# Kernel tuning notes

Hardware: AMD Instinct MI355X
Metric: run time of the kernel (lower is better)

The kernel has to match this reference:

```python
import jax, jax.numpy as jnp
import numpy as np

B, S, D = 4, 2048, 1024
H = 16
DH = D // H          # 64
DFF = 4096
EPS = 1e-5


def _layer_norm(x, gamma, beta):
    mu = jnp.mean(x, axis=-1, keepdims=True)
    var = jnp.mean(jnp.square(x - mu), axis=-1, keepdims=True)
    return (x - mu) * jax.lax.rsqrt(var + EPS) * gamma + beta


def setup_inputs() -> dict:
    key = jax.random.key(0)
    ks = jax.random.split(key, 8)
    s_in = 1.0 / np.sqrt(D)
    s_ff = 1.0 / np.sqrt(DFF)
    return {
        "x": jax.random.normal(ks[0], (B, S, D), dtype=jnp.float32),
        # per-head qkv weights stacked: [H, D, 3*DH] (nn.Linear, bias=False)
        "Wqkv": jax.random.normal(ks[1], (H, D, 3 * DH), dtype=jnp.float32) * s_in,
        "Wproj": jax.random.normal(ks[2], (D, D), dtype=jnp.float32) * s_in,
        "bproj": jnp.zeros((D,), dtype=jnp.float32),
        "ln1_g": jnp.ones((D,), dtype=jnp.float32),
        "ln1_b": jnp.zeros((D,), dtype=jnp.float32),
        "ln2_g": jnp.ones((D,), dtype=jnp.float32),
        "ln2_b": jnp.zeros((D,), dtype=jnp.float32),
        "W1": jax.random.normal(ks[3], (D, DFF), dtype=jnp.float32) * s_in,
        "b1": jnp.zeros((DFF,), dtype=jnp.float32),
        "W2": jax.random.normal(ks[4], (DFF, D), dtype=jnp.float32) * s_ff,
        "b2": jnp.zeros((D,), dtype=jnp.float32),
    }


def reference(x, Wqkv, Wproj, bproj, ln1_g, ln1_b, ln2_g, ln2_b, W1, b1, W2, b2):
    # fused multi-head QKV projection: [B,S,D] x [H,D,3*DH] -> [B,H,S,3*DH]
    qkv = jnp.einsum('bsd,hde->bhse', x, Wqkv)
    q, k, v = jnp.split(qkv, 3, axis=-1)          # each [B,H,S,DH]
    scale = 1.0 / jnp.sqrt(jnp.asarray(DH, dtype=x.dtype))
    scores = jnp.einsum('bhsd,bhtd->bhst', q, k) * scale   # [B,H,S,S]
    causal = jnp.tril(jnp.ones((S, S), dtype=bool))
    scores = jnp.where(causal, scores, jnp.finfo(x.dtype).min)
    attn = jax.nn.softmax(scores, axis=-1)
    heads = jnp.einsum('bhst,bhtd->bhsd', attn, v)          # [B,H,S,DH]
    att_out = heads.transpose(0, 2, 1, 3).reshape(B, S, D)  # concat heads
    att_out = att_out @ Wproj + bproj
    out = _layer_norm(x + att_out, ln1_g, ln1_b)            # dropout = identity (eval)
    mlp_out = (jax.nn.gelu(out @ W1 + b1, approximate=False)) @ W2 + b2
    out = _layer_norm(out + mlp_out, ln2_g, ln2_b)
    return out
```

## Files before the change

kernel.cpp:

```cpp
#include <hip/hip_runtime.h>
#include <math.h>

#define BB 4
#define SS 2048
#define DD 1024
#define HH 16
#define DHH 64
#define DFF 4096
static constexpr float LN_EPS = 1e-5f;

typedef __bf16 bf16x8 __attribute__((ext_vector_type(8)));
typedef float f32x4 __attribute__((ext_vector_type(4)));
typedef unsigned short u16x8 __attribute__((ext_vector_type(8)));

__device__ inline unsigned short f2bf(float f) {
    union { float f; unsigned int u; } v; v.f = f;
    unsigned int u = v.u + 0x7FFFu + ((v.u >> 16) & 1u);
    return (unsigned short)(u >> 16);
}

__device__ __forceinline__ float fexp2(float x) {
    return __builtin_amdgcn_exp2f(x);
}

__device__ __forceinline__ void gl_lds16(const unsigned short* g,
                                         unsigned short* l) {
    __builtin_amdgcn_global_load_lds(
        (const __attribute__((address_space(1))) unsigned int*)g,
        (__attribute__((address_space(3))) unsigned int*)l, 16, 0, 0);
}

__global__ __launch_bounds__(256) void transpose_bf16_kernel(
    const float* __restrict__ in, unsigned short* __restrict__ outT,
    int R, int C) {
    __shared__ float t[64][65];
    const int r0 = blockIdx.y * 64, c0 = blockIdx.x * 64;
    const int cl = threadIdx.x & 63, rl = threadIdx.x >> 6;
#pragma unroll
    for (int rr = 0; rr < 16; ++rr)
        t[rl + rr * 4][cl] = in[(size_t)(r0 + rl + rr * 4) * C + c0 + cl];
    __syncthreads();
#pragma unroll
    for (int rr = 0; rr < 16; ++rr)
        outT[(size_t)(c0 + rl + rr * 4) * R + r0 + cl] = f2bf(t[cl][rl + rr * 4]);
}

__global__ __launch_bounds__(256) void repack_wqkv_bf16_kernel(
    const float* __restrict__ Wqkv, unsigned short* __restrict__ Wq2T) {
    __shared__ float t[64][65];
    const int h = blockIdx.z;
    const int d0 = blockIdx.y * 64, e0 = blockIdx.x * 64;
    const int cl = threadIdx.x & 63, rl = threadIdx.x >> 6;
#pragma unroll
    for (int rr = 0; rr < 16; ++rr)
        t[rl + rr * 4][cl] =
            Wqkv[((size_t)h * DD + d0 + rl + rr * 4) * 192 + e0 + cl];
    __syncthreads();
#pragma unroll
    for (int rr = 0; rr < 16; ++rr)
        Wq2T[((size_t)h * 192 + e0 + rl + rr * 4) * DD + d0 + cl] =
            f2bf(t[cl][rl + rr * 4]);
}

__global__ __launch_bounds__(256) void f2bf_kernel(
    const float* __restrict__ in, unsigned short* __restrict__ out, int n) {
    int i = blockIdx.x * 256 + threadIdx.x;
    if (i < n) out[i] = f2bf(in[i]);
}

template <int MODE>
__global__ __launch_bounds__(256) void mfma_gemm_kernel(
    const unsigned short* __restrict__ A, const unsigned short* __restrict__ BT,
    float* __restrict__ Cf, unsigned short* __restrict__ Cb,
    const float* __restrict__ bias, const float* __restrict__ resid,
    unsigned short* __restrict__ Qb, unsigned short* __restrict__ Kb,
    unsigned short* __restrict__ VTb, int M, int N, int K) {
    __shared__ __align__(16) unsigned short lds_g[128 * 32 * 2];
    unsigned short* Als = lds_g;
    unsigned short* Bls = lds_g + 128 * 32;
    const int tid = threadIdx.x;
    const int lane = tid & 63;
    const int wave = tid >> 6;
    const int wr = (wave >> 1) * 64;
    const int wc = (wave & 1) * 64;
    const int row0 = blockIdx.y * 128;
    const int col0 = blockIdx.x * 128;

    const int lr = tid >> 2;
    const int lsl = (tid & 3) * 8;
    const int lkg = (((tid & 3) ^ ((lr >> 1) & 3)) * 8);
    const int l15 = lane & 15;
    const int g = lane >> 4;
    const int fk = ((g ^ ((l15 >> 1) & 3)) * 8);

    f32x4 acc[4][4] = {};

    for (int k0 = 0; k0 < K; k0 += 32) {
        __syncthreads();
        gl_lds16(&A[(size_t)(row0 + lr) * K + k0 + lkg], &Als[lr * 32 + lsl]);
        gl_lds16(&A[(size_t)(row0 + 64 + lr) * K + k0 + lkg],
                 &Als[(64 + lr) * 32 + lsl]);
        gl_lds16(&BT[(size_t)(col0 + lr) * K + k0 + lkg], &Bls[lr * 32 + lsl]);
        gl_lds16(&BT[(size_t)(col0 + 64 + lr) * K + k0 + lkg],
                 &Bls[(64 + lr) * 32 + lsl]);
        __syncthreads();

        bf16x8 af[4], bfr[4];
#pragma unroll
        for (int i = 0; i < 4; ++i)
            af[i] = __builtin_bit_cast(
                bf16x8, *(const u16x8*)&Als[(wr + i * 16 + l15) * 32 + fk]);
#pragma unroll
        for (int j = 0; j < 4; ++j)
            bfr[j] = __builtin_bit_cast(
                bf16x8, *(const u16x8*)&Bls[(wc + j * 16 + l15) * 32 + fk]);
#pragma unroll
        for (int i = 0; i < 4; ++i)
#pragma unroll
            for (int j = 0; j < 4; ++j)
                acc[i][j] = __builtin_amdgcn_mfma_f32_16x16x32_bf16(
                    af[i], bfr[j], acc[i][j], 0, 0, 0);
    }

    const int r_base = (lane >> 4) * 4;
    const int c_off = l15;

    if (MODE == 2) {
        const int slab = (wave >> 1) * 16 + r_base;
#pragma unroll
        for (int i = 0; i < 4; ++i) {
            __syncthreads();
#pragma unroll
            for (int j = 0; j < 4; ++j) {
                const int col = wc + j * 16 + c_off;
                const float bv = bias[col0 + col];
#pragma unroll
                for (int r = 0; r < 4; ++r) {
                    float v = acc[i][j][r] + bv;
                    float t = fexp2(v * (2.30211849f + 0.10294198f * v * v));
                    float gel = v * t * __builtin_amdgcn_rcpf(t + 1.f);
                    lds_g[(slab + r) * 136 + col] = f2bf(gel);
                }
            }
            __syncthreads();
#pragma unroll
            for (int it = 0; it < 2; ++it) {
                const int id = it * 256 + tid;
                const int sl = id >> 4, cc = (id & 15) * 8;
                const int row_g = row0 + ((sl < 16) ? (i * 16 + sl)
                                                    : (48 + i * 16 + sl));
                *(u16x8*)&Cb[(size_t)row_g * N + col0 + cc] =
                    *(const u16x8*)&lds_g[sl * 136 + cc];
            }
        }
        return;
    }

#pragma unroll
    for (int i = 0; i < 4; ++i) {
#pragma unroll
        for (int j = 0; j < 4; ++j) {
            const int col = col0 + wc + j * 16 + c_off;
            const int rowb = row0 + wr + i * 16 + r_base;
            if (MODE == 4) {
                const int h = col / 192, e = col % 192;
                const int bb = rowb >> 11, s = rowb & 2047;
                if (e < 64) {
                    unsigned short* q =
                        Qb + (((size_t)bb * HH + h) * SS + s) * 64 + e;
#pragma unroll
                    for (int r = 0; r < 4; ++r)
                        q[r * 64] = f2bf(acc[i][j][r] * 0.18033688f);
                } else if (e < 128) {
                    unsigned short* kp =
                        Kb + (((size_t)bb * HH + h) * SS + s) * 64 + (e - 64);
#pragma unroll
                    for (int r = 0; r < 4; ++r)
                        kp[r * 64] = f2bf(acc[i][j][r]);
                } else {
                    ushort4 pk;
                    pk.x = f2bf(acc[i][j][0]);
                    pk.y = f2bf(acc[i][j][1]);
                    pk.z = f2bf(acc[i][j][2]);
                    pk.w = f2bf(acc[i][j][3]);
                    *(ushort4*)(VTb + (((size_t)bb * HH + h) * 64 + (e - 128)) *
                                          SS + s) = pk;
                }
            } else {
                const float bv = bias[col];
#pragma unroll
                for (int r = 0; r < 4; ++r) {
                    const int row = rowb + r;
                    float v = acc[i][j][r] + bv + resid[(size_t)row * N + col];
                    Cf[(size_t)row * N + col] = v;
                }
            }
        }
    }
}

__global__ __launch_bounds__(256) void fattn_kernel(
    const unsigned short* __restrict__ Qb, const unsigned short* __restrict__ Kb,
    const unsigned short* __restrict__ VTb, unsigned short* __restrict__ att) {
    constexpr int QSTR = 68, KSTR = 68, VSTR = 76, PSTR = 68;
    __shared__ __align__(16) unsigned short Pls[128 * PSTR];
    __shared__ __align__(16) unsigned short Kls[64 * KSTR];
    __shared__ __align__(16) unsigned short VTls[64 * VSTR];

    const int bh = blockIdx.x;
    const int q0 = blockIdx.y * 128;
    const int tid = threadIdx.x;
    const int lane = tid & 63;
    const int wave = tid >> 6;
    const int l15 = lane & 15;
    const int g = lane >> 4;
    const int b = bh >> 4, h = bh & 15;

    const unsigned short* Qh = Qb + (size_t)bh * SS * 64;
    const unsigned short* Kh = Kb + (size_t)bh * SS * 64;
    const unsigned short* Vh = VTb + (size_t)bh * 64 * SS;

    {
        const int row = tid >> 1, c0 = (tid & 1) * 32;
        const unsigned short* src = Qh + (size_t)(q0 + row) * 64 + c0;
        unsigned short* dst = &Pls[row * QSTR + c0];
#pragma unroll
        for (int c = 0; c < 32; c += 8)
            *(u16x8*)(dst + c) = *(const u16x8*)(src + c);
    }
    __syncthreads();
    bf16x8 qf[2][2];
#pragma unroll
    for (int i = 0; i < 2; ++i)
#pragma unroll
        for (int ks = 0; ks < 2; ++ks)
            qf[i][ks] = __builtin_bit_cast(
                bf16x8, *(const u16x8*)&Pls[(wave * 32 + i * 16 + l15) * QSTR +
                                            ks * 32 + g * 8]);
    __syncthreads();

    f32x4 oacc[4][2] = {};
    float mst[2], lst[2];
#pragma unroll
    for (int i = 0; i < 2; ++i) { mst[i] = -1e30f; lst[i] = 0.f; }

    const int srow = tid >> 2, sc0 = (tid & 3) * 16;
    const int qlim = q0 + wave * 32 + 31;
    const int qrow = wave * 32 + l15;

    for (int t0 = 0; t0 <= q0 + 64; t0 += 64) {
        __syncthreads();
        {
            const unsigned short* ksrc = Kh + (size_t)(t0 + srow) * 64 + sc0;
            *(u16x8*)&Kls[srow * KSTR + sc0]     = *(const u16x8*)ksrc;
            *(u16x8*)&Kls[srow * KSTR + sc0 + 8] = *(const u16x8*)(ksrc + 8);
            const unsigned short* vsrc = Vh + (size_t)srow * SS + t0 + sc0;
            *(u16x8*)&VTls[srow * VSTR + sc0]     = *(const u16x8*)vsrc;
            *(u16x8*)&VTls[srow * VSTR + sc0 + 8] = *(const u16x8*)(vsrc + 8);
        }
        __syncthreads();
        if (t0 > qlim) continue;

        f32x4 sacc[4][2] = {};
#pragma unroll
        for (int ks = 0; ks < 2; ++ks) {
            bf16x8 kb[4];
#pragma unroll
            for (int j = 0; j < 4; ++j)
                kb[j] = __builtin_bit_cast(
                    bf16x8, *(const u16x8*)&Kls[(j * 16 + l15) * KSTR +
                                                ks * 32 + g * 8]);
#pragma unroll
            for (int j = 0; j < 4; ++j)
#pragma unroll
                for (int i = 0; i < 2; ++i)
                    sacc[j][i] = __builtin_amdgcn_mfma_f32_16x16x32_bf16(
                        kb[j], qf[i][ks], sacc[j][i], 0, 0, 0);
        }

        if (t0 >= q0) {
#pragma unroll
            for (int j = 0; j < 4; ++j)
#pragma unroll
                for (int i = 0; i < 2; ++i)
#pragma unroll
                    for (int r = 0; r < 4; ++r) {
                        const int kg = t0 + j * 16 + g * 4 + r;
                        const int qg = q0 + qrow + i * 16;
                        if (kg > qg) sacc[j][i][r] = -1e30f;
                    }
        }

#pragma unroll
        for (int i = 0; i < 2; ++i) {
            float mx = -1e30f;
#pragma unroll
            for (int j = 0; j < 4; ++j)
#pragma unroll
                for (int r = 0; r < 4; ++r) mx = fmaxf(mx, sacc[j][i][r]);
            mx = fmaxf(mx, __shfl_xor(mx, 16));
            mx = fmaxf(mx, __shfl_xor(mx, 32));
            const float mn = fmaxf(mst[i], mx);
            const float al = fexp2(mst[i] - mn);
            mst[i] = mn;
            float rsum = 0.f;
            const int pbase = (qrow + i * 16) * PSTR + g * 4;
#pragma unroll
            for (int j = 0; j < 4; ++j) {
                float p0 = fexp2(sacc[j][i][0] - mn);
                float p1 = fexp2(sacc[j][i][1] - mn);
                float p2 = fexp2(sacc[j][i][2] - mn);
                float p3 = fexp2(sacc[j][i][3] - mn);
                rsum += (p0 + p1) + (p2 + p3);
                ushort4 pk;
                pk.x = f2bf(p0); pk.y = f2bf(p1);
                pk.z = f2bf(p2); pk.w = f2bf(p3);
                *(ushort4*)&Pls[pbase + j * 16] = pk;
            }
            rsum += __shfl_xor(rsum, 16);
            rsum += __shfl_xor(rsum, 32);
            lst[i] = lst[i] * al + rsum;
#pragma unroll
            for (int jo = 0; jo < 4; ++jo)
#pragma unroll
                for (int r = 0; r < 4; ++r) oacc[jo][i][r] *= al;
        }
        __syncthreads();

#pragma unroll
        for (int ks = 0; ks < 2; ++ks) {
            bf16x8 vb[4], pf[2];
#pragma unroll
            for (int jo = 0; jo < 4; ++jo)
                vb[jo] = __builtin_bit_cast(
                    bf16x8, *(const u16x8*)&VTls[(jo * 16 + l15) * VSTR +
                                                 ks * 32 + g * 8]);
#pragma unroll
            for (int i = 0; i < 2; ++i)
                pf[i] = __builtin_bit_cast(
                    bf16x8, *(const u16x8*)&Pls[(qrow + i * 16) * PSTR +
                                                ks * 32 + g * 8]);
#pragma unroll
            for (int jo = 0; jo < 4; ++jo)
#pragma unroll
                for (int i = 0; i < 2; ++i)
                    oacc[jo][i] = __builtin_amdgcn_mfma_f32_16x16x32_bf16(
                        vb[jo], pf[i], oacc[jo][i], 0, 0, 0);
        }
    }

#pragma unroll
    for (int i = 0; i < 2; ++i) {
        const float inv = 1.f / lst[i];
        const int qg = q0 + qrow + i * 16;
        unsigned short* dst = att + ((size_t)b * SS + qg) * DD + h * 64 + g * 4;
#pragma unroll
        for (int jo = 0; jo < 4; ++jo) {
            ushort4 pk;
            pk.x = f2bf(oacc[jo][i][0] * inv);
            pk.y = f2bf(oacc[jo][i][1] * inv);
            pk.z = f2bf(oacc[jo][i][2] * inv);
            pk.w = f2bf(oacc[jo][i][3] * inv);
            *(ushort4*)(dst + jo * 16) = pk;
        }
    }
}

__global__ __launch_bounds__(256) void ln_kernel(
    const float* __restrict__ X, const float* __restrict__ g,
    const float* __restrict__ bta, float* __restrict__ Y,
    unsigned short* __restrict__ Yb) {
    const int row = blockIdx.x;
    const float4 xv = ((const float4*)(X + (size_t)row * DD))[threadIdx.x];

    __shared__ float red1[4], red2[4];
    float s = xv.x + xv.y + xv.z + xv.w;
#pragma unroll
    for (int off = 32; off > 0; off >>= 1) s += __shfl_down(s, off);
    const int wave = threadIdx.x >> 6;
    if ((threadIdx.x & 63) == 0) red1[wave] = s;
    __syncthreads();
    const float mu = (red1[0] + red1[1] + red1[2] + red1[3]) * (1.f / DD);

    float dx = xv.x - mu, dy = xv.y - mu, dz = xv.z - mu, dw = xv.w - mu;
    float s2 = dx * dx + dy * dy + dz * dz + dw * dw;
#pragma unroll
    for (int off = 32; off > 0; off >>= 1) s2 += __shfl_down(s2, off);
    if ((threadIdx.x & 63) == 0) red2[wave] = s2;
    __syncthreads();
    const float var = (red2[0] + red2[1] + red2[2] + red2[3]) * (1.f / DD);
    const float rstd = rsqrtf(var + LN_EPS);

    const float4 gv = ((const float4*)g)[threadIdx.x];
    const float4 bv = ((const float4*)bta)[threadIdx.x];
    float4 yv;
    yv.x = dx * rstd * gv.x + bv.x;
    yv.y = dy * rstd * gv.y + bv.y;
    yv.z = dz * rstd * gv.z + bv.z;
    yv.w = dw * rstd * gv.w + bv.w;
    ((float4*)(Y + (size_t)row * DD))[threadIdx.x] = yv;
    if (Yb) {
        ushort4 q;
        q.x = f2bf(yv.x); q.y = f2bf(yv.y);
        q.z = f2bf(yv.z); q.w = f2bf(yv.w);
        ((ushort4*)(Yb + (size_t)row * DD))[threadIdx.x] = q;
    }
}

extern "C" void kernel_launch(void* const* d_in, const int* in_sizes, int n_in,
                              void* d_out, int out_size, void* d_ws,
                              size_t ws_size, hipStream_t stream) {
    const float* x     = (const float*)d_in[0];
    const float* Wqkv  = (const float*)d_in[1];
    const float* Wproj = (const float*)d_in[2];
    const float* bproj = (const float*)d_in[3];
    const float* ln1_g = (const float*)d_in[4];
    const float* ln1_b = (const float*)d_in[5];
    const float* ln2_g = (const float*)d_in[6];
    const float* ln2_b = (const float*)d_in[7];
    const float* W1    = (const float*)d_in[8];
    const float* b1    = (const float*)d_in[9];
    const float* W2    = (const float*)d_in[10];
    const float* b2    = (const float*)d_in[11];
    float* out = (float*)d_out;

    const size_t M = (size_t)BB * SS;
    const size_t MB = 1024 * 1024;
    char* w = (char*)d_ws;
    unsigned short* Qb     = (unsigned short*)(w + 0);
    unsigned short* out1b  = (unsigned short*)(w + 0);
    unsigned short* Kb     = (unsigned short*)(w + 16 * MB);
    unsigned short* VTb    = (unsigned short*)(w + 32 * MB);
    unsigned short* hbuf   = (unsigned short*)(w + 16 * MB);
    unsigned short* Wq2T   = (unsigned short*)(w + 96 * MB);
    unsigned short* xb     = (unsigned short*)(w + 102 * MB);
    unsigned short* att    = (unsigned short*)(w + 96 * MB);
    float*          out1   = (float*)(w + 96 * MB);
    unsigned short* WprojT = (unsigned short*)(w + 118 * MB);
    unsigned short* W1T    = (unsigned short*)(w + 128 * MB);
    unsigned short* W2T    = (unsigned short*)(w + 136 * MB);

    repack_wqkv_bf16_kernel<<<dim3(3, 16, 16), 256, 0, stream>>>(Wqkv, Wq2T);
    transpose_bf16_kernel<<<dim3(16, 16), 256, 0, stream>>>(Wproj, WprojT, 1024, 1024);
    transpose_bf16_kernel<<<dim3(64, 16), 256, 0, stream>>>(W1, W1T, 1024, 4096);
    transpose_bf16_kernel<<<dim3(16, 64), 256, 0, stream>>>(W2, W2T, 4096, 1024);
    f2bf_kernel<<<(int)((M * DD + 255) / 256), 256, 0, stream>>>(x, xb, (int)(M * DD));

    mfma_gemm_kernel<4><<<dim3(3072 / 128, M / 128), 256, 0, stream>>>(
        xb, Wq2T, nullptr, nullptr, nullptr, nullptr, Qb, Kb, VTb,
        (int)M, 3072, 1024);

    fattn_kernel<<<dim3(BB * HH, SS / 128), 256, 0, stream>>>(Qb, Kb, VTb, att);

    mfma_gemm_kernel<3><<<dim3(1024 / 128, M / 128), 256, 0, stream>>>(
        att, WprojT, out, nullptr, bproj, x, nullptr, nullptr, nullptr,
        (int)M, 1024, 1024);

    ln_kernel<<<(int)M, 256, 0, stream>>>(out, ln1_g, ln1_b, out1, out1b);

    mfma_gemm_kernel<2><<<dim3(4096 / 128, M / 128), 256, 0, stream>>>(
        out1b, W1T, nullptr, hbuf, b1, nullptr, nullptr, nullptr, nullptr,
        (int)M, 4096, 1024);

    mfma_gemm_kernel<3><<<dim3(1024 / 128, M / 128), 256, 0, stream>>>(
        hbuf, W2T, out, nullptr, b2, out1, nullptr, nullptr, nullptr,
        (int)M, 1024, 4096);

    ln_kernel<<<(int)M, 256, 0, stream>>>(out, ln2_g, ln2_b, out, nullptr);
}
```

Measured before the change: 585.5 us.

## Replace 128x128 GEMM with 256x256 ping-pong pipelined MFMA kernel

Swaps the simple 128x128-tile, single-buffered GEMM for a 512-thread, 256x256-tile kernel. It uses a BK=64 double-buffered LDS pipeline split into quarter-tiles, interleaving async global-to-LDS loads with MFMA quads under explicit barriers and vmcnt waits. It also adds XOR swizzled LDS layout, s_setprio around MFMA bursts, and a workgroup-index swizzle for L2 locality. The aim is to raise arithmetic intensity and hide memory latency. In exchange it uses 128KB LDS and large accumulator register pressure, and fewer blocks run on the small N=1024 GEMMs.

```diff
diff --git a/kernel.cpp b/kernel.cpp
--- a/kernel.cpp
+++ b/kernel.cpp
@@ -30,6 +30,14 @@
         (__attribute__((address_space(3))) unsigned int*)l, 16, 0, 0);
 }
 
+#define GBAR()                               \
+    do {                                     \
+        asm volatile("" ::: "memory");       \
+        __builtin_amdgcn_s_barrier();        \
+        asm volatile("" ::: "memory");       \
+    } while (0)
+#define VMCNT(n) asm volatile("s_waitcnt vmcnt(" #n ")" ::: "memory")
+
 __global__ __launch_bounds__(256) void transpose_bf16_kernel(
     const float* __restrict__ in, unsigned short* __restrict__ outT,
     int R, int C) {
@@ -68,100 +76,199 @@
     if (i < n) out[i] = f2bf(in[i]);
 }
 
+__device__ __forceinline__ void read_afrag(const unsigned short* s, int base,
+                                           int wm, int l15, int g,
+                                           bf16x8 af[4][2]) {
+#pragma unroll
+    for (int ii = 0; ii < 4; ++ii) {
+        const int lr = wm * 64 + ii * 16 + l15;
+#pragma unroll
+        for (int ks = 0; ks < 2; ++ks) {
+            const int p = ((ks << 2) + g) ^ (lr & 7);
+            af[ii][ks] = __builtin_bit_cast(
+                bf16x8, *(const u16x8*)&s[base + lr * 64 + p * 8]);
+        }
+    }
+}
+
+__device__ __forceinline__ void read_bfrag(const unsigned short* s, int base,
+                                           int wn, int l15, int g,
+                                           bf16x8 bf2[2][2]) {
+#pragma unroll
+    for (int jj = 0; jj < 2; ++jj) {
+        const int lr = wn * 32 + jj * 16 + l15;
+#pragma unroll
+        for (int ks = 0; ks < 2; ++ks) {
+            const int p = ((ks << 2) + g) ^ (lr & 7);
+            bf2[jj][ks] = __builtin_bit_cast(
+                bf16x8, *(const u16x8*)&s[base + lr * 64 + p * 8]);
+        }
+    }
+}
+
+template <int RS>
+__device__ __forceinline__ void stage_half(const unsigned short* __restrict__ G,
+                                           int ldK, int growbase, int kbase,
+                                           unsigned short* lbase, int tid) {
+#pragma unroll
+    for (int s = 0; s < 2; ++s) {
+        const int c16 = s * 512 + tid;
+        const int r = c16 >> 3, c = c16 & 7;
+        const int grow =
+            growbase + ((r >> RS) << (RS + 1)) + (r & ((1 << RS) - 1));
+        const int gcol = kbase + ((c ^ (r & 7)) << 3);
+        gl_lds16(&G[(size_t)grow * ldK + gcol], &lbase[c16 << 3]);
+    }
+}
+
+template <int MH, int NH>
+__device__ __forceinline__ void mfma_quad(f32x4 acc[8][4],
+                                          const bf16x8 af[4][2],
+                                          const bf16x8 bf2[2][2]) {
+    __builtin_amdgcn_s_setprio(1);
+#pragma unroll
+    for (int ks = 0; ks < 2; ++ks)
+#pragma unroll
+        for (int ii = 0; ii < 4; ++ii)
+#pragma unroll
+            for (int jj = 0; jj < 2; ++jj)
+                acc[MH * 4 + ii][NH * 2 + jj] =
+                    __builtin_amdgcn_mfma_f32_16x16x32_bf16(
+                        af[ii][ks], bf2[jj][ks],
+                        acc[MH * 4 + ii][NH * 2 + jj], 0, 0, 0);
+    __builtin_amdgcn_s_setprio(0);
+}
+
 template <int MODE>
-__global__ __launch_bounds__(256) void mfma_gemm_kernel(
+__global__ __launch_bounds__(512) void mfma_gemm256_kernel(
     const unsigned short* __restrict__ A, const unsigned short* __restrict__ BT,
     float* __restrict__ Cf, unsigned short* __restrict__ Cb,
     const float* __restrict__ bias, const float* __restrict__ resid,
     unsigned short* __restrict__ Qb, unsigned short* __restrict__ Kb,
     unsigned short* __restrict__ VTb, int M, int N, int K) {
-    __shared__ __align__(16) unsigned short lds_g[128 * 32 * 2];
-    unsigned short* Als = lds_g;
-    unsigned short* Bls = lds_g + 128 * 32;
+    __shared__ __align__(16) unsigned short smem[65536];
     const int tid = threadIdx.x;
-    const int lane = tid & 63;
-    const int wave = tid >> 6;
-    const int wr = (wave >> 1) * 64;
-    const int wc = (wave & 1) * 64;
-    const int row0 = blockIdx.y * 128;
-    const int col0 = blockIdx.x * 128;
-
-    const int lr = tid >> 2;
-    const int lsl = (tid & 3) * 8;
-    const int lkg = (((tid & 3) ^ ((lr >> 1) & 3)) * 8);
-    const int l15 = lane & 15;
-    const int g = lane >> 4;
-    const int fk = ((g ^ ((l15 >> 1) & 3)) * 8);
-
-    f32x4 acc[4][4] = {};
-
-    for (int k0 = 0; k0 < K; k0 += 32) {
-        __syncthreads();
-        gl_lds16(&A[(size_t)(row0 + lr) * K + k0 + lkg], &Als[lr * 32 + lsl]);
-        gl_lds16(&A[(size_t)(row0 + 64 + lr) * K + k0 + lkg],
-                 &Als[(64 + lr) * 32 + lsl]);
-        gl_lds16(&BT[(size_t)(col0 + lr) * K + k0 + lkg], &Bls[lr * 32 + lsl]);
-        gl_lds16(&BT[(size_t)(col0 + 64 + lr) * K + k0 + lkg],
-                 &Bls[(64 + lr) * 32 + lsl]);
-        __syncthreads();
-
-        bf16x8 af[4], bfr[4];
-#pragma unroll
-        for (int i = 0; i < 4; ++i)
-            af[i] = __builtin_bit_cast(
-                bf16x8, *(const u16x8*)&Als[(wr + i * 16 + l15) * 32 + fk]);
-#pragma unroll
-        for (int j = 0; j < 4; ++j)
-            bfr[j] = __builtin_bit_cast(
-                bf16x8, *(const u16x8*)&Bls[(wc + j * 16 + l15) * 32 + fk]);
-#pragma unroll
-        for (int i = 0; i < 4; ++i)
-#pragma unroll
-            for (int j = 0; j < 4; ++j)
-                acc[i][j] = __builtin_amdgcn_mfma_f32_16x16x32_bf16(
-                    af[i], bfr[j], acc[i][j], 0, 0, 0);
-    }
-
-    const int r_base = (lane >> 4) * 4;
-    const int c_off = l15;
+    const int lane = tid & 63, wave = tid >> 6;
+    const int wm = wave >> 2, wn = wave & 3;
+    const int l15 = lane & 15, g = lane >> 4;
+
+    const int gx = gridDim.x, nwg = gx * gridDim.y;
+    const int lid = blockIdx.y * gx + blockIdx.x;
+    const int swz = ((nwg & 7) == 0) ? ((lid & 7) * (nwg >> 3) + (lid >> 3))
+                                     : lid;
+    const int row0 = (swz / gx) * 256;
+    const int col0 = (swz % gx) * 256;
+
+    const int kt = K >> 6;
+
+    f32x4 acc[8][4] = {};
+
+    stage_half<6>(A, K, row0, 0, smem + 0, tid);
+    stage_half<6>(A, K, row0 + 64, 0, smem + 8192, tid);
+    stage_half<5>(BT, K, col0, 0, smem + 32768, tid);
+    stage_half<5>(BT, K, col0 + 32, 0, smem + 40960, tid);
+    VMCNT(4);
+    stage_half<6>(A, K, row0, 64, smem + 16384, tid);
+    stage_half<6>(A, K, row0 + 64, 64, smem + 24576, tid);
+    stage_half<5>(BT, K, col0, 64, smem + 49152, tid);
+    VMCNT(6);
+    GBAR();
+
+    bf16x8 af[4][2], bf0[2][2], bf1[2][2];
+    for (int it = 0; it < (kt >> 1); ++it) {
+        const int t1k = (2 * it + 1) << 6;
+        int t2 = 2 * it + 2; if (t2 > kt - 1) t2 = kt - 1;
+        int t3 = 2 * it + 3; if (t3 > kt - 1) t3 = kt - 1;
+        const int t2k = t2 << 6, t3k = t3 << 6;
+
+        read_afrag(smem, 0, wm, l15, g, af);
+        read_bfrag(smem, 32768, wn, l15, g, bf0);
+        stage_half<5>(BT, K, col0 + 32, t1k, smem + 57344, tid);
+        GBAR();
+        mfma_quad<0, 0>(acc, af, bf0);
+        GBAR();
+
+        read_bfrag(smem, 40960, wn, l15, g, bf1);
+        stage_half<6>(A, K, row0, t2k, smem + 0, tid);
+        GBAR();
+        mfma_quad<0, 1>(acc, af, bf1);
+        GBAR();
+
+        read_afrag(smem, 8192, wm, l15, g, af);
+        stage_half<5>(BT, K, col0, t2k, smem + 32768, tid);
+        GBAR();
+        mfma_quad<1, 1>(acc, af, bf1);
+        GBAR();
+
+        stage_half<6>(A, K, row0 + 64, t2k, smem + 8192, tid);
+        GBAR();
+        mfma_quad<1, 0>(acc, af, bf0);
+        VMCNT(6);
+        GBAR();
+
+        read_afrag(smem, 16384, wm, l15, g, af);
+        read_bfrag(smem, 49152, wn, l15, g, bf0);
+        stage_half<5>(BT, K, col0 + 32, t2k, smem + 40960, tid);
+        GBAR();
+        mfma_quad<0, 0>(acc, af, bf0);
+        GBAR();
+
+        read_bfrag(smem, 57344, wn, l15, g, bf1);
+        stage_half<6>(A, K, row0, t3k, smem + 16384, tid);
+        GBAR();
+        mfma_quad<0, 1>(acc, af, bf1);
+        GBAR();
+
+        read_afrag(smem, 24576, wm, l15, g, af);
+        stage_half<5>(BT, K, col0, t3k, smem + 49152, tid);
+        GBAR();
+        mfma_quad<1, 1>(acc, af, bf1);
+        GBAR();
+
+        stage_half<6>(A, K, row0 + 64, t3k, smem + 24576, tid);
+        GBAR();
+        mfma_quad<1, 0>(acc, af, bf0);
+        VMCNT(6);
+        GBAR();
+    }
+    VMCNT(0);
+    GBAR();
 
     if (MODE == 2) {
-        const int slab = (wave >> 1) * 16 + r_base;
-#pragma unroll
-        for (int i = 0; i < 4; ++i) {
+        constexpr int SLAB = 264;
+#pragma unroll
+        for (int i2 = 0; i2 < 8; ++i2) {
             __syncthreads();
 #pragma unroll
-            for (int j = 0; j < 4; ++j) {
-                const int col = wc + j * 16 + c_off;
+            for (int j2 = 0; j2 < 4; ++j2) {
+                const int col = wn * 64 + j2 * 16 + l15;
                 const float bv = bias[col0 + col];
 #pragma unroll
                 for (int r = 0; r < 4; ++r) {
-                    float v = acc[i][j][r] + bv;
+                    float v = acc[i2][j2][r] + bv;
                     float t = fexp2(v * (2.30211849f + 0.10294198f * v * v));
                     float gel = v * t * __builtin_amdgcn_rcpf(t + 1.f);
-                    lds_g[(slab + r) * 136 + col] = f2bf(gel);
+                    smem[(wm * 16 + g * 4 + r) * SLAB + col] = f2bf(gel);
                 }
             }
             __syncthreads();
-#pragma unroll
-            for (int it = 0; it < 2; ++it) {
-                const int id = it * 256 + tid;
-                const int sl = id >> 4, cc = (id & 15) * 8;
-                const int row_g = row0 + ((sl < 16) ? (i * 16 + sl)
-                                                    : (48 + i * 16 + sl));
-                *(u16x8*)&Cb[(size_t)row_g * N + col0 + cc] =
-                    *(const u16x8*)&lds_g[sl * 136 + cc];
-            }
+            const int sr = tid >> 4;
+            const int cc = (tid & 15) * 16;
+            const int grow = row0 + ((sr >> 4) << 7) + i2 * 16 + (sr & 15);
+            *(u16x8*)&Cb[(size_t)grow * N + col0 + cc] =
+                *(const u16x8*)&smem[sr * SLAB + cc];
+            *(u16x8*)&Cb[(size_t)grow * N + col0 + cc + 8] =
+                *(const u16x8*)&smem[sr * SLAB + cc + 8];
         }
         return;
     }
 
 #pragma unroll
-    for (int i = 0; i < 4; ++i) {
-#pragma unroll
-        for (int j = 0; j < 4; ++j) {
-            const int col = col0 + wc + j * 16 + c_off;
-            const int rowb = row0 + wr + i * 16 + r_base;
+    for (int i2 = 0; i2 < 8; ++i2) {
+#pragma unroll
+        for (int j2 = 0; j2 < 4; ++j2) {
+            const int col = col0 + wn * 64 + j2 * 16 + l15;
+            const int rowb = row0 + wm * 128 + i2 * 16 + g * 4;
             if (MODE == 4) {
                 const int h = col / 192, e = col % 192;
                 const int bb = rowb >> 11, s = rowb & 2047;
@@ -170,19 +277,19 @@
                         Qb + (((size_t)bb * HH + h) * SS + s) * 64 + e;
 #pragma unroll
                     for (int r = 0; r < 4; ++r)
-                        q[r * 64] = f2bf(acc[i][j][r] * 0.18033688f);
+                        q[r * 64] = f2bf(acc[i2][j2][r] * 0.18033688f);
                 } else if (e < 128) {
                     unsigned short* kp =
                         Kb + (((size_t)bb * HH + h) * SS + s) * 64 + (e - 64);
 #pragma unroll
                     for (int r = 0; r < 4; ++r)
-                        kp[r * 64] = f2bf(acc[i][j][r]);
+                        kp[r * 64] = f2bf(acc[i2][j2][r]);
                 } else {
                     ushort4 pk;
-                    pk.x = f2bf(acc[i][j][0]);
-                    pk.y = f2bf(acc[i][j][1]);
-                    pk.z = f2bf(acc[i][j][2]);
-                    pk.w = f2bf(acc[i][j][3]);
+                    pk.x = f2bf(acc[i2][j2][0]);
+                    pk.y = f2bf(acc[i2][j2][1]);
+                    pk.z = f2bf(acc[i2][j2][2]);
+                    pk.w = f2bf(acc[i2][j2][3]);
                     *(ushort4*)(VTb + (((size_t)bb * HH + h) * 64 + (e - 128)) *
                                           SS + s) = pk;
                 }
@@ -191,7 +298,7 @@
 #pragma unroll
                 for (int r = 0; r < 4; ++r) {
                     const int row = rowb + r;
-                    float v = acc[i][j][r] + bv + resid[(size_t)row * N + col];
+                    float v = acc[i2][j2][r] + bv + resid[(size_t)row * N + col];
                     Cf[(size_t)row * N + col] = v;
                 }
             }
@@ -446,23 +553,23 @@
     transpose_bf16_kernel<<<dim3(16, 64), 256, 0, stream>>>(W2, W2T, 4096, 1024);
     f2bf_kernel<<<(int)((M * DD + 255) / 256), 256, 0, stream>>>(x, xb, (int)(M * DD));
 
-    mfma_gemm_kernel<4><<<dim3(3072 / 128, M / 128), 256, 0, stream>>>(
+    mfma_gemm256_kernel<4><<<dim3(3072 / 256, M / 256), 512, 0, stream>>>(
         xb, Wq2T, nullptr, nullptr, nullptr, nullptr, Qb, Kb, VTb,
         (int)M, 3072, 1024);
 
     fattn_kernel<<<dim3(BB * HH, SS / 128), 256, 0, stream>>>(Qb, Kb, VTb, att);
 
-    mfma_gemm_kernel<3><<<dim3(1024 / 128, M / 128), 256, 0, stream>>>(
+    mfma_gemm256_kernel<3><<<dim3(1024 / 256, M / 256), 512, 0, stream>>>(
         att, WprojT, out, nullptr, bproj, x, nullptr, nullptr, nullptr,
         (int)M, 1024, 1024);
 
     ln_kernel<<<(int)M, 256, 0, stream>>>(out, ln1_g, ln1_b, out1, out1b);
 
-    mfma_gemm_kernel<2><<<dim3(4096 / 128, M / 128), 256, 0, stream>>>(
+    mfma_gemm256_kernel<2><<<dim3(4096 / 256, M / 256), 512, 0, stream>>>(
         out1b, W1T, nullptr, hbuf, b1, nullptr, nullptr, nullptr, nullptr,
         (int)M, 4096, 1024);
 
-    mfma_gemm_kernel<3><<<dim3(1024 / 128, M / 128), 256, 0, stream>>>(
+    mfma_gemm256_kernel<3><<<dim3(1024 / 256, M / 256), 512, 0, stream>>>(
         hbuf, W2T, out, nullptr, b2, out1, nullptr, nullptr, nullptr,
         (int)M, 1024, 4096);
 
```

Result: faster. 553.9 us (-5.4%).
